# Performance work log

Measured on AMD Instinct MI355X. Metric: run time of the kernel, lower is better.

## Reference

```python
import jax, jax.numpy as jnp
import numpy as np

B, T, D = 4, 8192, 768
H, K, V = 12, 64, 64
EPS_RMS = 1e-6
EPS_NORM = 1e-12  # F.normalize default eps


def setup_inputs() -> dict:
    key = jax.random.key(0)
    ks = jax.random.split(key, 7)
    s = 1.0 / np.sqrt(D)
    return {
        "x": jax.random.normal(ks[0], (B, T, D), jnp.float32),
        "w_norm": jnp.ones((D,), jnp.float32),
        "Wk": jax.random.normal(ks[1], (D, H * K), jnp.float32) * s,   # stored [in,out]
        "Wv": jax.random.normal(ks[2], (D, H * V), jnp.float32) * s,
        "Wo": jax.random.normal(ks[3], (H * V, D), jnp.float32) * (1.0 / np.sqrt(H * V)),
        "Wb": jax.random.normal(ks[4], (D, H), jnp.float32) * s,
        "bb": jnp.full((H,), -2.0, jnp.float32),  # delta_beta_init
        "Wg": jax.random.normal(ks[5], (D, H), jnp.float32) * s,
        "bg": jnp.full((H,), 2.0, jnp.float32),   # delta_g_init
    }


def reference(x, w_norm, Wk, Wv, Wo, Wb, bb, Wg, bg):
    Bx, Tx, Dx = x.shape
    # RMSNorm
    xn = x * jax.lax.rsqrt(jnp.mean(x * x, axis=-1, keepdims=True) + EPS_RMS) * w_norm
    k = (xn @ Wk).reshape(Bx, Tx, H, K)
    v = (xn @ Wv).reshape(Bx, Tx, H, V)
    beta = jax.nn.sigmoid(xn @ Wb + bb)  # [B,T,H]
    g = jax.nn.sigmoid(xn @ Wg + bg)     # [B,T,H]
    # L2-normalize keys along head dim (F.normalize, p=2)
    k = k / jnp.maximum(jnp.linalg.norm(k, axis=-1, keepdims=True), EPS_NORM)

    def step(state, inp):
        # state: [B,H,K,V]
        k_t, v_t, b_t, g_t = inp  # [B,H,K],[B,H,V],[B,H],[B,H]
        pred = jnp.einsum('bhkv,bhk->bhv', state, k_t)
        err = v_t - pred
        state = g_t[..., None, None] * state + b_t[..., None, None] * (
            k_t[..., None] * err[:, :, None, :])
        out_t = jnp.einsum('bhkv,bhk->bhv', state, k_t)
        return state, out_t

    init = jnp.zeros((Bx, H, K, V), x.dtype)
    xs = (jnp.swapaxes(k, 0, 1), jnp.swapaxes(v, 0, 1),
          jnp.swapaxes(beta, 0, 1), jnp.swapaxes(g, 0, 1))
    final_state, outs = jax.lax.scan(step, init, xs)  # outs: [T,B,H,V]
    delta = jnp.swapaxes(outs, 0, 1).reshape(Bx, Tx, H * V) @ Wo
    out = x + delta
    return out, final_state
```

## Files before the change

### kernel.cpp

```cpp
#include <hip/hip_runtime.h>
#include <hip/hip_bf16.h>


typedef __attribute__((ext_vector_type(8))) short short8;
typedef __attribute__((ext_vector_type(4))) float floatx4;

#define DEVFN static __device__ __forceinline__

typedef const __attribute__((address_space(1))) unsigned int* as1_u32p;
typedef __attribute__((address_space(3))) unsigned int* as3_u32p;

DEVFN void gll16(const void* g, void* l) {
  __builtin_amdgcn_global_load_lds((as1_u32p)g, (as3_u32p)l, 16, 0, 0);
}

DEVFN unsigned short f2bf_u(float f) {
  __hip_bfloat16 h = __float2bfloat16(f);
  return __builtin_bit_cast(unsigned short, h);
}
DEVFN float bf2f(unsigned short u) {
  return __bfloat162float(__builtin_bit_cast(__hip_bfloat16, u));
}

static constexpr int T_LEN = 8192;
static constexpr int ROWS  = 4 * 8192;
static constexpr int D     = 768;
static constexpr int NKV   = 1664;
static constexpr int NC    = 128;
static constexpr int NBH   = 48;
static constexpr int NWG1  = NBH * NC;
static constexpr int NG    = 16;
static constexpr int NGRP  = NBH * NG;
static constexpr int CSTR  = 192;

DEVFN int swz16(int row, int slot) {
  return (row << 7) + (((slot ^ (row & 7)) & 7) << 4);
}
DEVFN int swzE(int row, int col) {
  return (row << 7) + ((((col >> 3) ^ (row & 7)) & 7) << 4) + ((col & 7) << 1);
}
DEVFN void st_bf(char* base, int row, int col, float v) {
  *(unsigned short*)(base + swzE(row, col)) = f2bf_u(v);
}
DEVFN float ld_bf(const char* base, int row, int col) {
  return bf2f(*(const unsigned short*)(base + swzE(row, col)));
}
DEVFN void mm16x64(const char* aB, const char* bB, int wv, int lane, floatx4 acc[4]) {
  #pragma unroll
  for (int ks = 0; ks < 2; ++ks) {
    short8 af = *(const short8*)(aB + swz16(wv * 16 + (lane & 15), ks * 4 + (lane >> 4)));
    #pragma unroll
    for (int t = 0; t < 4; ++t) {
      short8 bf = *(const short8*)(bB + swz16(t * 16 + (lane & 15), ks * 4 + (lane >> 4)));
      acc[t] = __builtin_amdgcn_mfma_f32_16x16x32_bf16(af, bf, acc[t], 0, 0, 0);
    }
  }
}

__global__ void k_prep_wt(const float* __restrict__ Wk, const float* __restrict__ Wv,
                          const float* __restrict__ Wb, const float* __restrict__ Wg,
                          __hip_bfloat16* __restrict__ WT) {
  int idx = blockIdx.x * 256 + threadIdx.x;
  if (idx >= NKV * D) return;
  int n = idx / D, k = idx % D;
  float v;
  if (n < 768)       v = Wk[k * 768 + n];
  else if (n < 1536) v = Wv[k * 768 + (n - 768)];
  else if (n < 1548) v = Wb[k * 12 + (n - 1536)];
  else if (n < 1560) v = Wg[k * 12 + (n - 1548)];
  else               v = 0.f;
  WT[idx] = __float2bfloat16(v);
}

__global__ void k_prep_wo(const float* __restrict__ Wo, __hip_bfloat16* __restrict__ WoT) {
  int idx = blockIdx.x * 256 + threadIdx.x;
  int n = idx / D, k = idx % D;
  WoT[idx] = __float2bfloat16(Wo[k * 768 + n]);
}

__global__ void k_rmsnorm(const float* __restrict__ x, const float* __restrict__ wn,
                          __hip_bfloat16* __restrict__ xn) {
  int wid  = (blockIdx.x << 2) + (threadIdx.x >> 6);
  int lane = threadIdx.x & 63;
  const float* xr = x + (size_t)wid * D;
  float4 a = *(const float4*)(xr + lane * 4);
  float4 b = *(const float4*)(xr + 256 + lane * 4);
  float4 c = *(const float4*)(xr + 512 + lane * 4);
  float ss = a.x*a.x + a.y*a.y + a.z*a.z + a.w*a.w
           + b.x*b.x + b.y*b.y + b.z*b.z + b.w*b.w
           + c.x*c.x + c.y*c.y + c.z*c.z + c.w*c.w;
  #pragma unroll
  for (int m = 1; m < 64; m <<= 1) ss += __shfl_xor(ss, m);
  float rs = rsqrtf(ss * (1.f / 768.f) + 1e-6f);
  float4 w0 = *(const float4*)(wn + lane * 4);
  float4 w1 = *(const float4*)(wn + 256 + lane * 4);
  float4 w2 = *(const float4*)(wn + 512 + lane * 4);
  unsigned short* xo = (unsigned short*)(xn + (size_t)wid * D);
  ushort4 u;
  u.x = f2bf_u(a.x*rs*w0.x); u.y = f2bf_u(a.y*rs*w0.y); u.z = f2bf_u(a.z*rs*w0.z); u.w = f2bf_u(a.w*rs*w0.w);
  *(ushort4*)(xo + lane * 4) = u;
  u.x = f2bf_u(b.x*rs*w1.x); u.y = f2bf_u(b.y*rs*w1.y); u.z = f2bf_u(b.z*rs*w1.z); u.w = f2bf_u(b.w*rs*w1.w);
  *(ushort4*)(xo + 256 + lane * 4) = u;
  u.x = f2bf_u(c.x*rs*w2.x); u.y = f2bf_u(c.y*rs*w2.y); u.z = f2bf_u(c.z*rs*w2.z); u.w = f2bf_u(c.w*rs*w2.w);
  *(ushort4*)(xo + 512 + lane * 4) = u;
}

template <int EPI>
__global__ __launch_bounds__(256)
void k_gemm(const __hip_bfloat16* __restrict__ A, const __hip_bfloat16* __restrict__ Bt,
            __hip_bfloat16* __restrict__ Ck, __hip_bfloat16* __restrict__ Cv,
            float* __restrict__ Cbg, float* __restrict__ C0, const float* __restrict__ Xadd) {
  __shared__ __align__(16) unsigned short As[2][128 * 64];
  __shared__ __align__(16) unsigned short Bs[2][128 * 64];
  const int K = 768, NKT = 12;
  int tid = threadIdx.x, lane = tid & 63, w = tid >> 6;
  int wr = w >> 1, wc = w & 1;
  int bx = blockIdx.x;
  bx = (bx & 7) * 32 + (bx >> 3);
  int m0 = bx * 128, n0 = blockIdx.y * 128;
  floatx4 zero = {0.f, 0.f, 0.f, 0.f};
  floatx4 acc[4][4];
  #pragma unroll
  for (int i = 0; i < 4; ++i)
    #pragma unroll
    for (int j = 0; j < 4; ++j) acc[i][j] = zero;

  auto stage = [&](int buf, int kt) {
    #pragma unroll
    for (int it = 0; it < 4; ++it) {
      int L = it * 256 + tid;
      int r = L >> 3, s = L & 7, sg = s ^ (r & 7);
      gll16(A  + (size_t)(m0 + r) * K + kt * 64 + sg * 8, &As[buf][L * 8]);
      gll16(Bt + (size_t)(n0 + r) * K + kt * 64 + sg * 8, &Bs[buf][L * 8]);
    }
  };

  stage(0, 0);
  __syncthreads();
  int buf = 0;
  for (int kt = 0; kt < NKT; ++kt) {
    if (kt + 1 < NKT) stage(buf ^ 1, kt + 1);
    __builtin_amdgcn_s_setprio(1);
    #pragma unroll
    for (int ks = 0; ks < 2; ++ks) {
      int c = ks * 4 + (lane >> 4);
      short8 af[4], bfr[4];
      #pragma unroll
      for (int i = 0; i < 4; ++i) {
        int ri = wr * 64 + i * 16 + (lane & 15);
        af[i] = *(const short8*)&As[buf][ri * 64 + ((c ^ (ri & 7)) << 3)];
      }
      #pragma unroll
      for (int j = 0; j < 4; ++j) {
        int rj = wc * 64 + j * 16 + (lane & 15);
        bfr[j] = *(const short8*)&Bs[buf][rj * 64 + ((c ^ (rj & 7)) << 3)];
      }
      #pragma unroll
      for (int i = 0; i < 4; ++i)
        #pragma unroll
        for (int j = 0; j < 4; ++j)
          acc[i][j] = __builtin_amdgcn_mfma_f32_16x16x32_bf16(af[i], bfr[j], acc[i][j], 0, 0, 0);
    }
    __builtin_amdgcn_s_setprio(0);
    __syncthreads();
    buf ^= 1;
  }

  if constexpr (EPI == 0) {
    if (n0 < 768) {
      #pragma unroll
      for (int i = 0; i < 4; ++i) {
        #pragma unroll
        for (int r = 0; r < 4; ++r) {
          float ss = 0.f;
          #pragma unroll
          for (int j = 0; j < 4; ++j) { float t = acc[i][j][r]; ss = fmaf(t, t, ss); }
          ss += __shfl_xor(ss, 1); ss += __shfl_xor(ss, 2);
          ss += __shfl_xor(ss, 4); ss += __shfl_xor(ss, 8);
          float sc = 1.f / fmaxf(sqrtf(ss), 1e-12f);
          int mm = m0 + wr * 64 + i * 16 + (lane >> 4) * 4 + r;
          #pragma unroll
          for (int j = 0; j < 4; ++j) {
            int n = n0 + wc * 64 + j * 16 + (lane & 15);
            Ck[(size_t)mm * 768 + n] = __float2bfloat16(acc[i][j][r] * sc);
          }
        }
      }
    } else if (n0 < 1536) {
      #pragma unroll
      for (int i = 0; i < 4; ++i)
        #pragma unroll
        for (int j = 0; j < 4; ++j) {
          int n = n0 + wc * 64 + j * 16 + (lane & 15) - 768;
          #pragma unroll
          for (int r = 0; r < 4; ++r) {
            int mm = m0 + wr * 64 + i * 16 + (lane >> 4) * 4 + r;
            Cv[(size_t)mm * 768 + n] = __float2bfloat16(acc[i][j][r]);
          }
        }
    } else {
      #pragma unroll
      for (int i = 0; i < 4; ++i)
        #pragma unroll
        for (int j = 0; j < 4; ++j) {
          int n = n0 + wc * 64 + j * 16 + (lane & 15) - 1536;
          #pragma unroll
          for (int r = 0; r < 4; ++r) {
            int mm = m0 + wr * 64 + i * 16 + (lane >> 4) * 4 + r;
            Cbg[(size_t)mm * 128 + n] = acc[i][j][r];
          }
        }
    }
  } else {
    #pragma unroll
    for (int i = 0; i < 4; ++i)
      #pragma unroll
      for (int j = 0; j < 4; ++j) {
        int n = n0 + wc * 64 + j * 16 + (lane & 15);
        #pragma unroll
        for (int r = 0; r < 4; ++r) {
          int mm = m0 + wr * 64 + i * 16 + (lane >> 4) * 4 + r;
          size_t o = (size_t)mm * 768 + n;
          C0[o] = Xadd[o] + acc[i][j][r];
        }
      }
  }
}

__global__ void k_gates2(const float* __restrict__ bgraw, const float* __restrict__ bb,
                         const float* __restrict__ bgb, float* __restrict__ csbuf) {
  int wid  = blockIdx.x * 4 + (threadIdx.x >> 6);
  int lane = threadIdx.x & 63;
  int bh = wid >> 7, ck = wid & 127;
  int b = bh / 12, h = bh % 12;
  size_t row0 = (size_t)b * T_LEN + (size_t)ck * 64;
  const float* br = bgraw + (row0 + lane) * 128;
  float bet = 1.f / (1.f + __expf(-(br[h] + bb[h])));
  float g   = 1.f / (1.f + __expf(-(br[12 + h] + bgb[h])));
  float lg = __log2f(g);
  float ci = lg;
  #pragma unroll
  for (int d = 1; d < 64; d <<= 1) { float t = __shfl_up(ci, d); if (lane >= d) ci += t; }
  csbuf[(size_t)wid * CSTR + lane] = ci;
  csbuf[(size_t)wid * CSTR + 64 + lane] = ci - lg;
  csbuf[(size_t)wid * CSTR + 128 + lane] = bet;
}

__global__ __launch_bounds__(256)
void k_chunk1(const __hip_bfloat16* __restrict__ kb16, const __hip_bfloat16* __restrict__ vbuf,
              const float* __restrict__ csbuf,
              __hip_bfloat16* __restrict__ Uvt_g, __hip_bfloat16* __restrict__ W_g) {
  __shared__ __align__(16) char sm[6 * 8192 + 768];
  char* SA = sm;
  char* SB = sm + 8192;
  char* SC = sm + 2 * 8192;
  char* SD = sm + 3 * 8192;
  char* SE = sm + 4 * 8192;
  char* SF = sm + 5 * 8192;
  float* cs   = (float*)(sm + 6 * 8192);
  float* cps  = (float*)(sm + 6 * 8192 + 256);
  float* bets = (float*)(sm + 6 * 8192 + 512);

  int blk = blockIdx.x, bh = blk >> 7, ck = blk & 127;
  int b = bh / 12, h = bh % 12;
  int tid = threadIdx.x, lane = tid & 63, wv = tid >> 6;
  size_t row0 = (size_t)b * T_LEN + (size_t)ck * 64;
  size_t wbase = (size_t)blk * 4096;

  if (tid < 64) {
    cs[tid]   = csbuf[(size_t)blk * CSTR + tid];
    cps[tid]  = csbuf[(size_t)blk * CSTR + 64 + tid];
    bets[tid] = csbuf[(size_t)blk * CSTR + 128 + tid];
  }
  int sr = tid >> 2, sc0 = (tid & 3) * 16;
  {
    const __hip_bfloat16* kp = kb16 + (row0 + sr) * 768 + h * 64 + sc0;
    short8 k0 = *(const short8*)kp;
    short8 k1 = *(const short8*)(kp + 8);
    *(short8*)(SA + swz16(sr, sc0 >> 3)) = k0;
    *(short8*)(SA + swz16(sr, (sc0 >> 3) + 1)) = k1;
  }
  short8 vreg0, vreg1;
  {
    const __hip_bfloat16* vp = vbuf + (row0 + sr) * 768 + h * 64 + sc0;
    vreg0 = *(const short8*)vp;
    vreg1 = *(const short8*)(vp + 8);
  }
  __syncthreads();

  floatx4 acc[4];
  auto zacc = [&] {
    #pragma unroll
    for (int t = 0; t < 4; ++t) acc[t] = (floatx4){0.f, 0.f, 0.f, 0.f};
  };
  auto forRC = [&](auto&& f) {
    #pragma unroll
    for (int t = 0; t < 4; ++t)
      #pragma unroll
      for (int r = 0; r < 4; ++r)
        f(wv * 16 + (lane >> 4) * 4 + r, t * 16 + (lane & 15), acc[t][r]);
  };

  zacc(); mm16x64(SA, SA, wv, lane, acc);
  forRC([&](int i, int j, float v) {
    float Lv = 0.f;
    if (j < i) Lv = bets[i] * exp2f(cps[i] - cs[j]) * v;
    st_bf(SB, i, j, Lv);
    st_bf(SC, j, i, Lv);
    st_bf(SD, i, j, (i == j ? 1.f : 0.f) - Lv);
  });
  __syncthreads();

  auto power = [&](char* Ar, char* Bt, char* Or, char* Ot) {
    zacc(); mm16x64(Ar, Bt, wv, lane, acc);
    forRC([&](int i, int j, float v) { st_bf(Or, i, j, v); st_bf(Ot, j, i, v); });
    __syncthreads();
  };
  auto powerT = [&](char* Ar, char* Bt, char* Ot) {
    zacc(); mm16x64(Ar, Bt, wv, lane, acc);
    forRC([&](int i, int j, float v) { st_bf(Ot, j, i, v); });
    __syncthreads();
  };
  auto combine = [&](char* Mr, char* Pt, char* Out) {
    zacc(); mm16x64(Mr, Pt, wv, lane, acc);
    forRC([&](int i, int j, float v) { st_bf(Out, i, j, v + ld_bf(Mr, i, j)); });
    __syncthreads();
  };

  power(SB, SC, SE, SF);
  combine(SD, SF, SB);
  power(SE, SF, SC, SD);
  combine(SB, SD, SE);
  power(SC, SD, SF, SB);
  combine(SE, SB, SC);
  power(SF, SB, SD, SE);
  combine(SC, SE, SF);
  powerT(SD, SE, SB);
  combine(SF, SB, SC);

  {
    float be = bets[sr];
    #pragma unroll
    for (int q = 0; q < 8; ++q) {
      st_bf(SD, sc0 + q,     sr, be * bf2f(((unsigned short*)&vreg0)[q]));
      st_bf(SD, sc0 + 8 + q, sr, be * bf2f(((unsigned short*)&vreg1)[q]));
    }
    float scl = be * exp2f(cps[sr]);
    #pragma unroll
    for (int q = 0; q < 16; ++q) {
      float kv = ld_bf(SA, sr, sc0 + q);
      st_bf(SD, 64 + sc0 + q, sr, scl * kv);
    }
  }
  __syncthreads();

  {
    floatx4 xacc[8];
    #pragma unroll
    for (int t = 0; t < 8; ++t) xacc[t] = (floatx4){0.f, 0.f, 0.f, 0.f};
    #pragma unroll
    for (int ks = 0; ks < 2; ++ks) {
      short8 af = *(const short8*)(SC + swz16(wv * 16 + (lane & 15), ks * 4 + (lane >> 4)));
      #pragma unroll
      for (int t = 0; t < 8; ++t) {
        short8 bf = *(const short8*)(SD + swz16(t * 16 + (lane & 15), ks * 4 + (lane >> 4)));
        xacc[t] = __builtin_amdgcn_mfma_f32_16x16x32_bf16(af, bf, xacc[t], 0, 0, 0);
      }
    }
    #pragma unroll
    for (int t = 0; t < 8; ++t) {
      int c = t * 16 + (lane & 15);
      #pragma unroll
      for (int r = 0; r < 4; ++r) {
        int i = wv * 16 + (lane >> 4) * 4 + r;
        float v = xacc[t][r];
        if (c < 64) st_bf(SF, c, i, v);
        else        W_g[wbase + (size_t)(c - 64) * 64 + i] = __float2bfloat16(v);
      }
    }
  }
  __syncthreads();

  {
    int s2 = (tid & 3) * 2;
    short8 a0 = *(const short8*)(SF + swz16(sr, s2));
    short8 a1 = *(const short8*)(SF + swz16(sr, s2 + 1));
    *(short8*)(Uvt_g + wbase + (size_t)sr * 64 + s2 * 8) = a0;
    *(short8*)(Uvt_g + wbase + (size_t)sr * 64 + s2 * 8 + 8) = a1;
  }
}

__global__ __launch_bounds__(256)
void k_scanA(const __hip_bfloat16* __restrict__ kb16, const __hip_bfloat16* __restrict__ W_g,
             const __hip_bfloat16* __restrict__ Uvt_g, const float* __restrict__ csbuf,
             __hip_bfloat16* __restrict__ Ag_g, __hip_bfloat16* __restrict__ Bg_g) {
  __shared__ __align__(16) char sm[7 * 8192];
  char* SK  = sm;
  char* SW  = sm + 8192;
  char* SU  = sm + 2 * 8192;
  char* SAc = sm + 3 * 8192;
  char* SBc = sm + 4 * 8192;
  char* SAt = sm + 5 * 8192;
  char* SBa = sm + 6 * 8192;

  int blk = blockIdx.x, bh = blk >> 4, gg = blk & 15;
  int b = bh / 12, h = bh % 12;
  int tid = threadIdx.x, lane = tid & 63, wv = tid >> 6;
  int sr = tid >> 2, sc0 = (tid & 3) * 16, s2 = (tid & 3) * 2;
  int c0 = gg * 8;

  short8 z = {0, 0, 0, 0, 0, 0, 0, 0};
  *(short8*)(SAt + swz16(sr, s2)) = z;
  *(short8*)(SAt + swz16(sr, s2 + 1)) = z;
  *(short8*)(SBa + swz16(sr, s2)) = z;
  *(short8*)(SBa + swz16(sr, s2 + 1)) = z;
  __syncthreads();
  if (tid < 64) st_bf(SAt, tid, tid, 1.f);

  floatx4 acc[4];
  auto zacc = [&] {
    #pragma unroll
    for (int t = 0; t < 4; ++t) acc[t] = (floatx4){0.f, 0.f, 0.f, 0.f};
  };
  auto forRC = [&](auto&& f) {
    #pragma unroll
    for (int t = 0; t < 4; ++t)
      #pragma unroll
      for (int r = 0; r < 4; ++r)
        f(wv * 16 + (lane >> 4) * 4 + r, t * 16 + (lane & 15), acc[t][r]);
  };

  for (int cc = 0; cc < 8; ++cc) {
    int c = c0 + cc;
    size_t row0 = (size_t)b * T_LEN + (size_t)c * 64;
    size_t wb = ((size_t)bh * NC + c) * 4096;
    const float* csb = csbuf + (size_t)(bh * NC + c) * CSTR;
    float cs_sr = csb[sr], cs63 = csb[63];
    const __hip_bfloat16* kp = kb16 + (row0 + sr) * 768 + h * 64 + sc0;
    short8 k0 = *(const short8*)kp, k1 = *(const short8*)(kp + 8);
    const __hip_bfloat16* wp = W_g + wb + (size_t)sr * 64 + s2 * 8;
    short8 w0 = *(const short8*)wp, w1 = *(const short8*)(wp + 8);
    const __hip_bfloat16* up = Uvt_g + wb + (size_t)sr * 64 + s2 * 8;
    short8 u0 = *(const short8*)up, u1 = *(const short8*)(up + 8);
    float scl = exp2f(cs63 - cs_sr);
    #pragma unroll
    for (int q = 0; q < 8; ++q) {
      st_bf(SK, sc0 + q,     sr, scl * bf2f(((unsigned short*)&k0)[q]));
      st_bf(SK, sc0 + 8 + q, sr, scl * bf2f(((unsigned short*)&k1)[q]));
    }
    *(short8*)(SW + swz16(sr, s2)) = w0;
    *(short8*)(SW + swz16(sr, s2 + 1)) = w1;
    *(short8*)(SU + swz16(sr, s2)) = u0;
    *(short8*)(SU + swz16(sr, s2 + 1)) = u1;
    __syncthreads();
    float gC = exp2f(cs63);
    zacc(); mm16x64(SW, SK, wv, lane, acc);
    forRC([&](int i, int j, float v) { st_bf(SAc, j, i, ((i == j) ? gC : 0.f) - v); });
    zacc(); mm16x64(SU, SK, wv, lane, acc);
    forRC([&](int i, int j, float v) { st_bf(SBc, i, j, v); });
    __syncthreads();
    zacc(); mm16x64(SAt, SAc, wv, lane, acc);
    forRC([&](int i, int j, float v) { st_bf(SAt, i, j, v); });
    zacc(); mm16x64(SBa, SAc, wv, lane, acc);
    forRC([&](int i, int j, float v) { st_bf(SBa, i, j, v + ld_bf(SBc, i, j)); });
  }
  __syncthreads();
  size_t gb = (size_t)blk * 4096;
  #pragma unroll
  for (int q = 0; q < 16; ++q)
    Ag_g[gb + (size_t)(sc0 + q) * 64 + sr] = __float2bfloat16(ld_bf(SAt, sr, sc0 + q));
  {
    short8 b0 = *(const short8*)(SBa + swz16(sr, s2));
    short8 b1 = *(const short8*)(SBa + swz16(sr, s2 + 1));
    *(short8*)(Bg_g + gb + (size_t)sr * 64 + s2 * 8) = b0;
    *(short8*)(Bg_g + gb + (size_t)sr * 64 + s2 * 8 + 8) = b1;
  }
}

__global__ __launch_bounds__(256)
void k_scanB(const __hip_bfloat16* __restrict__ Ag_g, const __hip_bfloat16* __restrict__ Bg_g,
             __hip_bfloat16* __restrict__ Sg_g, float* __restrict__ fstate) {
  __shared__ __align__(16) char sm[3 * 8192];
  char* SSt = sm;
  char* SAg = sm + 8192;
  char* SBg = sm + 2 * 8192;
  int bh = blockIdx.x;
  int tid = threadIdx.x, lane = tid & 63, wv = tid >> 6;
  int sr = tid >> 2, s2 = (tid & 3) * 2;

  short8 z = {0, 0, 0, 0, 0, 0, 0, 0};
  *(short8*)(SSt + swz16(sr, s2)) = z;
  *(short8*)(SSt + swz16(sr, s2 + 1)) = z;

  floatx4 acc[4];
  for (int g = 0; g < NG; ++g) {
    size_t gb = ((size_t)bh * NG + g) * 4096;
    const __hip_bfloat16* pa = Ag_g + gb + (size_t)sr * 64 + s2 * 8;
    short8 a0 = *(const short8*)pa, a1 = *(const short8*)(pa + 8);
    const __hip_bfloat16* pb = Bg_g + gb + (size_t)sr * 64 + s2 * 8;
    short8 b0 = *(const short8*)pb, b1 = *(const short8*)(pb + 8);
    __syncthreads();
    {
      short8 s0 = *(const short8*)(SSt + swz16(sr, s2));
      short8 s1 = *(const short8*)(SSt + swz16(sr, s2 + 1));
      *(short8*)(Sg_g + gb + (size_t)sr * 64 + s2 * 8) = s0;
      *(short8*)(Sg_g + gb + (size_t)sr * 64 + s2 * 8 + 8) = s1;
    }
    *(short8*)(SAg + swz16(sr, s2)) = a0;
    *(short8*)(SAg + swz16(sr, s2 + 1)) = a1;
    *(short8*)(SBg + swz16(sr, s2)) = b0;
    *(short8*)(SBg + swz16(sr, s2 + 1)) = b1;
    __syncthreads();
    #pragma unroll
    for (int t = 0; t < 4; ++t) acc[t] = (floatx4){0.f, 0.f, 0.f, 0.f};
    mm16x64(SSt, SAg, wv, lane, acc);
    #pragma unroll
    for (int t = 0; t < 4; ++t) {
      int j = t * 16 + (lane & 15);
      #pragma unroll
      for (int r = 0; r < 4; ++r) {
        int i = wv * 16 + (lane >> 4) * 4 + r;
        float val = acc[t][r] + ld_bf(SBg, i, j);
        st_bf(SSt, i, j, val);
        if (g == NG - 1) fstate[(size_t)bh * 4096 + (size_t)j * 64 + i] = val;
      }
    }
  }
}

__global__ __launch_bounds__(256)
void k_scfuse(const __hip_bfloat16* __restrict__ kb16, const __hip_bfloat16* __restrict__ W_g,
              const __hip_bfloat16* __restrict__ Uvt_g, const float* __restrict__ csbuf,
              const __hip_bfloat16* __restrict__ Sg_g, __hip_bfloat16* __restrict__ outs) {
  __shared__ __align__(16) char sm[7 * 8192];
  char* SSt = sm;
  char* SKr = sm + 8192;
  char* SKt = sm + 2 * 8192;
  char* SW  = sm + 3 * 8192;
  char* SU  = sm + 4 * 8192;
  char* SAc = sm + 5 * 8192;
  char* SBc = sm + 6 * 8192;

  int blk = blockIdx.x, bh = blk >> 4, gg = blk & 15;
  int b = bh / 12, h = bh % 12;
  int tid = threadIdx.x, lane = tid & 63, wv = tid >> 6;
  int sr = tid >> 2, sc0 = (tid & 3) * 16, s2 = (tid & 3) * 2;
  int c0 = gg * 8;
  int iR0 = wv * 16 + (lane >> 4) * 4;

  {
    const __hip_bfloat16* sp = Sg_g + (size_t)blk * 4096 + (size_t)sr * 64 + s2 * 8;
    short8 s0 = *(const short8*)sp, s1 = *(const short8*)(sp + 8);
    *(short8*)(SSt + swz16(sr, s2)) = s0;
    *(short8*)(SSt + swz16(sr, s2 + 1)) = s1;
  }

  floatx4 acc[4], pAcc[4];
  auto zacc = [&] {
    #pragma unroll
    for (int t = 0; t < 4; ++t) acc[t] = (floatx4){0.f, 0.f, 0.f, 0.f};
  };
  auto forRC = [&](auto&& f) {
    #pragma unroll
    for (int t = 0; t < 4; ++t)
      #pragma unroll
      for (int r = 0; r < 4; ++r)
        f(iR0 + r, t * 16 + (lane & 15), acc[t][r]);
  };

  for (int cc = 0; cc < 8; ++cc) {
    int c = c0 + cc;
    size_t row0 = (size_t)b * T_LEN + (size_t)c * 64;
    size_t wb = ((size_t)bh * NC + c) * 4096;
    const float* csb = csbuf + (size_t)(bh * NC + c) * CSTR;
    float cs_sr = csb[sr], cs63 = csb[63];
    float csI[4], csJ[4];
    #pragma unroll
    for (int r = 0; r < 4; ++r) csI[r] = csb[iR0 + r];
    #pragma unroll
    for (int t = 0; t < 4; ++t) csJ[t] = csb[t * 16 + (lane & 15)];
    const __hip_bfloat16* kp = kb16 + (row0 + sr) * 768 + h * 64 + sc0;
    short8 k0 = *(const short8*)kp, k1 = *(const short8*)(kp + 8);
    const __hip_bfloat16* wp = W_g + wb + (size_t)sr * 64 + sc0;
    short8 w0 = *(const short8*)wp, w1 = *(const short8*)(wp + 8);
    const __hip_bfloat16* up = Uvt_g + wb + (size_t)sr * 64 + sc0;
    short8 u0 = *(const short8*)up, u1 = *(const short8*)(up + 8);
    __syncthreads();
    *(short8*)(SKr + swz16(sr, sc0 >> 3)) = k0;
    *(short8*)(SKr + swz16(sr, (sc0 >> 3) + 1)) = k1;
    {
      float scl = exp2f(cs63 - cs_sr);
      #pragma unroll
      for (int q = 0; q < 8; ++q) {
        st_bf(SKt, sc0 + q,     sr, scl * bf2f(((unsigned short*)&k0)[q]));
        st_bf(SKt, sc0 + 8 + q, sr, scl * bf2f(((unsigned short*)&k1)[q]));
      }
    }
    *(short8*)(SW + swz16(sr, s2)) = w0;
    *(short8*)(SW + swz16(sr, s2 + 1)) = w1;
    *(short8*)(SU + swz16(sr, s2)) = u0;
    *(short8*)(SU + swz16(sr, s2 + 1)) = u1;
    __syncthreads();
    float gC = exp2f(cs63);
    zacc(); mm16x64(SW, SKt, wv, lane, acc);
    forRC([&](int i, int j, float v) { st_bf(SAc, j, i, ((i == j) ? gC : 0.f) - v); });
    zacc(); mm16x64(SU, SKt, wv, lane, acc);
    forRC([&](int i, int j, float v) { st_bf(SBc, i, j, v); });
    __syncthreads();
    #pragma unroll
    for (int q = 0; q < 8; ++q) {
      st_bf(SW, sc0 + q,     sr, bf2f(((unsigned short*)&w0)[q]));
      st_bf(SW, sc0 + 8 + q, sr, bf2f(((unsigned short*)&w1)[q]));
    }
    zacc(); mm16x64(SKr, SKr, wv, lane, acc);
    #pragma unroll
    for (int t = 0; t < 4; ++t) {
      int j = t * 16 + (lane & 15);
      #pragma unroll
      for (int r = 0; r < 4; ++r) {
        int i = iR0 + r;
        float gs = (j <= i) ? exp2f(csI[r] - csJ[t]) * acc[t][r] : 0.f;
        st_bf(SKt, i, j, gs);
      }
    }
    __syncthreads();
    #pragma unroll
    for (int t = 0; t < 4; ++t) pAcc[t] = (floatx4){0.f, 0.f, 0.f, 0.f};
    mm16x64(SKr, SSt, wv, lane, pAcc);
    zacc(); mm16x64(SSt, SW, wv, lane, acc);
    forRC([&](int i, int j, float v) { st_bf(SU, i, j, ld_bf(SU, i, j) - v); });
    __syncthreads();
    zacc(); mm16x64(SKt, SU, wv, lane, acc);
    #pragma unroll
    for (int t = 0; t < 4; ++t) {
      int vc = t * 16 + (lane & 15);
      #pragma unroll
      for (int r = 0; r < 4; ++r) {
        int i = iR0 + r;
        float o = exp2f(csI[r]) * pAcc[t][r] + acc[t][r];
        st_bf(SKr, i, vc, o);
      }
    }
    zacc(); mm16x64(SSt, SAc, wv, lane, acc);
    forRC([&](int i, int j, float v) { st_bf(SSt, i, j, v + ld_bf(SBc, i, j)); });
    __syncthreads();
    {
      short8 a0 = *(const short8*)(SKr + swz16(sr, s2));
      short8 a1 = *(const short8*)(SKr + swz16(sr, s2 + 1));
      __hip_bfloat16* op = outs + (row0 + sr) * 768 + h * 64 + s2 * 8;
      *(short8*)op = a0;
      *(short8*)(op + 8) = a1;
    }
  }
}

extern "C" void kernel_launch(void* const* d_in, const int* in_sizes, int n_in,
                              void* d_out, int out_size, void* d_ws, size_t ws_size,
                              hipStream_t stream) {
  (void)in_sizes; (void)n_in; (void)out_size; (void)ws_size;
  const float* x   = (const float*)d_in[0];
  const float* wn  = (const float*)d_in[1];
  const float* Wk  = (const float*)d_in[2];
  const float* Wv  = (const float*)d_in[3];
  const float* Wo  = (const float*)d_in[4];
  const float* Wb  = (const float*)d_in[5];
  const float* bb  = (const float*)d_in[6];
  const float* Wg  = (const float*)d_in[7];
  const float* bgb = (const float*)d_in[8];
  float* out = (float*)d_out;

  char* ws = (char*)d_ws;
  size_t off = 0;
  const size_t TILE = (size_t)NWG1 * 4096 * 2;
  const size_t GTILE = (size_t)NGRP * 4096 * 2;
  __hip_bfloat16* xn   = (__hip_bfloat16*)(ws + off);
  __hip_bfloat16* Uvt  = (__hip_bfloat16*)(ws + off); off += TILE;
  __hip_bfloat16* WT   = (__hip_bfloat16*)(ws + off); off += (size_t)NKV * D * 2;
  __hip_bfloat16* WoT  = (__hip_bfloat16*)(ws + off); off += (size_t)D * D * 2;
  __hip_bfloat16* kb16 = (__hip_bfloat16*)(ws + off); off += (size_t)ROWS * D * 2;
  __hip_bfloat16* vbuf = (__hip_bfloat16*)(ws + off);
  __hip_bfloat16* outsb= (__hip_bfloat16*)(ws + off); off += TILE;
  float* bgraw         = (float*)(ws + off);
  __hip_bfloat16* Ag_g = (__hip_bfloat16*)(ws + off);
  __hip_bfloat16* Bg_g = Ag_g + (size_t)NGRP * 4096;
  __hip_bfloat16* Sg_g = Bg_g + (size_t)NGRP * 4096;
  __hip_bfloat16* W_g  = Sg_g + (size_t)NGRP * 4096;
  off += 3 * GTILE + TILE;
  float* csbuf         = (float*)(ws + off);          off += (size_t)NWG1 * CSTR * 4;

  k_prep_wt<<<(NKV * D + 255) / 256, 256, 0, stream>>>(Wk, Wv, Wb, Wg, WT);
  k_prep_wo<<<(D * D) / 256, 256, 0, stream>>>(Wo, WoT);
  k_rmsnorm<<<ROWS / 4, 256, 0, stream>>>(x, wn, xn);
  k_gemm<0><<<dim3(ROWS / 128, NKV / 128), 256, 0, stream>>>(xn, WT, kb16, vbuf, bgraw, nullptr, nullptr);
  k_gates2<<<NWG1 / 4, 256, 0, stream>>>(bgraw, bb, bgb, csbuf);
  k_chunk1<<<NWG1, 256, 0, stream>>>(kb16, vbuf, csbuf, Uvt, W_g);
  k_scanA<<<NGRP, 256, 0, stream>>>(kb16, W_g, Uvt, csbuf, Ag_g, Bg_g);
  k_scanB<<<NBH, 256, 0, stream>>>(Ag_g, Bg_g, Sg_g, out + (size_t)ROWS * D);
  k_scfuse<<<NGRP, 256, 0, stream>>>(kb16, W_g, Uvt, csbuf, Sg_g, outsb);
  k_gemm<1><<<dim3(ROWS / 128, D / 128), 256, 0, stream>>>(outsb, WoT, nullptr, nullptr, nullptr, out, x);
}
```

Measured before the change: 511.4 us.

## Triple-buffer GEMM K-loop, trim beta/g stores, drop a barrier in scan fuse

The projection GEMM moves from double to triple buffering of its LDS tiles, prefetching two K-tiles ahead. It replaces the full __syncthreads with a partial vmcnt wait plus a raw barrier, so global loads stay in flight across iterations. The beta/g epilogue now stores only the 24 live columns instead of all 128. In the chunked scan kernel, the transposed W copy and the gated Gram matrix get their own LDS buffers (SW2, SG), removing one block-wide barrier. This raises shared memory per block, which may lower occupancy.

```diff
diff --git a/kernel.cpp b/kernel.cpp
--- a/kernel.cpp
+++ b/kernel.cpp
@@ -110,8 +110,8 @@
 void k_gemm(const __hip_bfloat16* __restrict__ A, const __hip_bfloat16* __restrict__ Bt,
             __hip_bfloat16* __restrict__ Ck, __hip_bfloat16* __restrict__ Cv,
             float* __restrict__ Cbg, float* __restrict__ C0, const float* __restrict__ Xadd) {
-  __shared__ __align__(16) unsigned short As[2][128 * 64];
-  __shared__ __align__(16) unsigned short Bs[2][128 * 64];
+  __shared__ __align__(16) unsigned short As[3][128 * 64];
+  __shared__ __align__(16) unsigned short Bs[3][128 * 64];
   const int K = 768, NKT = 12;
   int tid = threadIdx.x, lane = tid & 63, w = tid >> 6;
   int wr = w >> 1, wc = w & 1;
@@ -136,10 +136,12 @@
   };
 
   stage(0, 0);
-  __syncthreads();
-  int buf = 0;
+  stage(1, 1);
+  asm volatile("s_waitcnt vmcnt(8)" ::: "memory");
+  __builtin_amdgcn_s_barrier();
   for (int kt = 0; kt < NKT; ++kt) {
-    if (kt + 1 < NKT) stage(buf ^ 1, kt + 1);
+    int cb = kt % 3;
+    if (kt + 2 < NKT) stage((kt + 2) % 3, kt + 2);
     __builtin_amdgcn_s_setprio(1);
     #pragma unroll
     for (int ks = 0; ks < 2; ++ks) {
@@ -148,12 +150,12 @@
       #pragma unroll
       for (int i = 0; i < 4; ++i) {
         int ri = wr * 64 + i * 16 + (lane & 15);
-        af[i] = *(const short8*)&As[buf][ri * 64 + ((c ^ (ri & 7)) << 3)];
+        af[i] = *(const short8*)&As[cb][ri * 64 + ((c ^ (ri & 7)) << 3)];
       }
       #pragma unroll
       for (int j = 0; j < 4; ++j) {
         int rj = wc * 64 + j * 16 + (lane & 15);
-        bfr[j] = *(const short8*)&Bs[buf][rj * 64 + ((c ^ (rj & 7)) << 3)];
+        bfr[j] = *(const short8*)&Bs[cb][rj * 64 + ((c ^ (rj & 7)) << 3)];
       }
       #pragma unroll
       for (int i = 0; i < 4; ++i)
@@ -162,8 +164,9 @@
           acc[i][j] = __builtin_amdgcn_mfma_f32_16x16x32_bf16(af[i], bfr[j], acc[i][j], 0, 0, 0);
     }
     __builtin_amdgcn_s_setprio(0);
-    __syncthreads();
-    buf ^= 1;
+    if (kt + 2 < NKT)      asm volatile("s_waitcnt vmcnt(8)" ::: "memory");
+    else if (kt + 1 < NKT) asm volatile("s_waitcnt vmcnt(0)" ::: "memory");
+    __builtin_amdgcn_s_barrier();
   }
 
   if constexpr (EPI == 0) {
@@ -204,10 +207,12 @@
         #pragma unroll
         for (int j = 0; j < 4; ++j) {
           int n = n0 + wc * 64 + j * 16 + (lane & 15) - 1536;
-          #pragma unroll
-          for (int r = 0; r < 4; ++r) {
-            int mm = m0 + wr * 64 + i * 16 + (lane >> 4) * 4 + r;
-            Cbg[(size_t)mm * 128 + n] = acc[i][j][r];
+          if (n < 24) {
+            #pragma unroll
+            for (int r = 0; r < 4; ++r) {
+              int mm = m0 + wr * 64 + i * 16 + (lane >> 4) * 4 + r;
+              Cbg[(size_t)mm * 128 + n] = acc[i][j][r];
+            }
           }
         }
     }
@@ -532,14 +537,16 @@
 void k_scfuse(const __hip_bfloat16* __restrict__ kb16, const __hip_bfloat16* __restrict__ W_g,
               const __hip_bfloat16* __restrict__ Uvt_g, const float* __restrict__ csbuf,
               const __hip_bfloat16* __restrict__ Sg_g, __hip_bfloat16* __restrict__ outs) {
-  __shared__ __align__(16) char sm[7 * 8192];
+  __shared__ __align__(16) char sm[9 * 8192];
   char* SSt = sm;
   char* SKr = sm + 8192;
   char* SKt = sm + 2 * 8192;
-  char* SW  = sm + 3 * 8192;
-  char* SU  = sm + 4 * 8192;
-  char* SAc = sm + 5 * 8192;
-  char* SBc = sm + 6 * 8192;
+  char* SG  = sm + 3 * 8192;
+  char* SW  = sm + 4 * 8192;
+  char* SW2 = sm + 5 * 8192;
+  char* SU  = sm + 6 * 8192;
+  char* SAc = sm + 7 * 8192;
+  char* SBc = sm + 8 * 8192;
 
   int blk = blockIdx.x, bh = blk >> 4, gg = blk & 15;
   int b = bh / 12, h = bh % 12;
@@ -598,6 +605,11 @@
     }
     *(short8*)(SW + swz16(sr, s2)) = w0;
     *(short8*)(SW + swz16(sr, s2 + 1)) = w1;
+    #pragma unroll
+    for (int q = 0; q < 8; ++q) {
+      st_bf(SW2, sc0 + q,     sr, bf2f(((unsigned short*)&w0)[q]));
+      st_bf(SW2, sc0 + 8 + q, sr, bf2f(((unsigned short*)&w1)[q]));
+    }
     *(short8*)(SU + swz16(sr, s2)) = u0;
     *(short8*)(SU + swz16(sr, s2 + 1)) = u1;
     __syncthreads();
@@ -606,12 +618,6 @@
     forRC([&](int i, int j, float v) { st_bf(SAc, j, i, ((i == j) ? gC : 0.f) - v); });
     zacc(); mm16x64(SU, SKt, wv, lane, acc);
     forRC([&](int i, int j, float v) { st_bf(SBc, i, j, v); });
-    __syncthreads();
-    #pragma unroll
-    for (int q = 0; q < 8; ++q) {
-      st_bf(SW, sc0 + q,     sr, bf2f(((unsigned short*)&w0)[q]));
-      st_bf(SW, sc0 + 8 + q, sr, bf2f(((unsigned short*)&w1)[q]));
-    }
     zacc(); mm16x64(SKr, SKr, wv, lane, acc);
     #pragma unroll
     for (int t = 0; t < 4; ++t) {
@@ -620,17 +626,17 @@
       for (int r = 0; r < 4; ++r) {
         int i = iR0 + r;
         float gs = (j <= i) ? exp2f(csI[r] - csJ[t]) * acc[t][r] : 0.f;
-        st_bf(SKt, i, j, gs);
+        st_bf(SG, i, j, gs);
       }
     }
     __syncthreads();
     #pragma unroll
     for (int t = 0; t < 4; ++t) pAcc[t] = (floatx4){0.f, 0.f, 0.f, 0.f};
     mm16x64(SKr, SSt, wv, lane, pAcc);
-    zacc(); mm16x64(SSt, SW, wv, lane, acc);
+    zacc(); mm16x64(SSt, SW2, wv, lane, acc);
     forRC([&](int i, int j, float v) { st_bf(SU, i, j, ld_bf(SU, i, j) - v); });
     __syncthreads();
-    zacc(); mm16x64(SKt, SU, wv, lane, acc);
+    zacc(); mm16x64(SG, SU, wv, lane, acc);
     #pragma unroll
     for (int t = 0; t < 4; ++t) {
       int vc = t * 16 + (lane & 15);
```

Result: slower. 621.4 us (+21.5%).
